# Kernel tuning notes

Hardware: AMD Instinct MI355X
Metric: run time of the kernel (lower is better)

## Reference

```python
import jax, jax.numpy as jnp
import numpy as np
from jax import lax

EPS = 0.1
MAX_ITER = 100
THRESH = 0.01
N = 4  # number of prompt ensembles


def _l2norm(x, axis):
    return x / jnp.linalg.norm(x, axis=axis, keepdims=True)


def sinkhorn(K, u, v, max_iter=MAX_ITER, thresh=THRESH):
    # K: [B, M, N], u: [B, M], v: [B, N]. Matches torch loop with early exit
    # on mean(|r - r0|) < thresh, done on-device via lax.while_loop.
    dt = K.dtype
    r0 = jnp.ones_like(u)
    c0 = jnp.ones_like(v)

    def cond(state):
        _, _, i, err = state
        return jnp.logical_and(i < max_iter, err >= thresh)

    def body(state):
        r, c, i, _ = state
        r_new = u / jnp.einsum('bmn,bn->bm', K, c)
        c_new = v / jnp.einsum('bmn,bm->bn', K, r_new)
        err = jnp.mean(jnp.abs(r_new - r))
        return (r_new, c_new, i + 1, err)

    r, c, _, _ = lax.while_loop(cond, body, (r0, c0, jnp.int32(0), jnp.asarray(jnp.inf, dt)))
    # T = outer(r, c) * K
    return r[:, :, None] * c[:, None, :] * K


def setup_inputs() -> dict:
    key = jax.random.key(0)
    k1, k2, k3 = jax.random.split(key, 3)
    M, b, d = 196, 32, 512
    n_cls = 1000
    return {
        'image_features': jax.random.normal(k1, (M, b, d), dtype=jnp.float32),
        'image_feature_pool': jax.random.normal(k2, (b, d), dtype=jnp.float32),
        'text_features': jax.random.normal(k3, (N * n_cls, d), dtype=jnp.float32),
        'logit_scale': jnp.asarray(np.log(1.0 / 0.07), dtype=jnp.float32),
    }


def reference(image_features, image_feature_pool, text_features, logit_scale):
    M, b, d = image_features.shape
    n_cls = text_features.shape[0] // N

    tf = text_features.reshape(N, n_cls, d)
    text_feature_pool = tf.mean(axis=0)

    imf = _l2norm(image_features, axis=2)          # [M, b, d]
    img_pool = _l2norm(image_feature_pool, axis=1)  # [b, d]
    tfn = _l2norm(tf, axis=2)                       # [N, n_cls, d]
    txt_pool = _l2norm(text_feature_pool, axis=1)   # [n_cls, d]

    # sim: [M, N, b, n_cls] -> [M, N, b*n_cls] -> [B, M, N]
    sim = jnp.einsum('mbd,ncd->mnbc', imf, tfn)
    sim = sim.reshape(M, N, b * n_cls).transpose(2, 0, 1)
    wdist = 1.0 - sim

    B = b * n_cls
    xx = jnp.full((B, M), 1.0 / M, dtype=sim.dtype)
    yy = jnp.full((B, N), 1.0 / N, dtype=sim.dtype)

    # torch.no_grad() around Sinkhorn -> stop gradients into the iteration
    K = jnp.exp(-lax.stop_gradient(wdist) / EPS)
    T = sinkhorn(K, xx, yy)

    sim_op = jnp.sum(T * sim, axis=(1, 2)).reshape(b, n_cls)

    ls = jnp.exp(logit_scale)
    logits = ls * (img_pool @ txt_pool.T)
    logits2 = 0.5 * (ls * sim_op) + 0.5 * logits
    return logits2
```

## Files before the change

### kernel.cpp

```cpp
#include <hip/hip_runtime.h>
#include <hip/hip_bf16.h>

#define MB 6272
#define NC 4000
#define DD 512
#define NCLS 1000
#define NB 32000
#define NITER 6
#define SK_STRIDE 68

typedef __attribute__((ext_vector_type(8))) short short8;
typedef __attribute__((ext_vector_type(4))) float f32x4;
typedef __attribute__((ext_vector_type(2))) float f32x2;

__device__ __forceinline__ float bflo(unsigned u) { return __builtin_bit_cast(float, u << 16); }
__device__ __forceinline__ float bfhi(unsigned u) { return __builtin_bit_cast(float, u & 0xFFFF0000u); }
__device__ __forceinline__ float frcp(float x) { return __builtin_amdgcn_rcpf(x); }

__device__ __forceinline__ unsigned short f2bf(float x) {
  unsigned u = __builtin_bit_cast(unsigned, x);
  u += 0x7FFFu + ((u >> 16) & 1u);
  return (unsigned short)(u >> 16);
}

__device__ __forceinline__ bool is_fp32_mode(const void* lsp) {
  const unsigned short u = *(const unsigned short*)lsp;
  const float v = __builtin_bit_cast(float, (unsigned)u << 16);
  return !(v > 2.55f && v < 2.77f);
}

__device__ __forceinline__ void gl_lds16(const unsigned short* g, unsigned short* l) {
  __builtin_amdgcn_global_load_lds(
      (const __attribute__((address_space(1))) void*)g,
      (__attribute__((address_space(3))) void*)l, 16, 0, 0);
}

__global__ __launch_bounds__(256) void prep(const void* __restrict__ imgf,
                                            const void* __restrict__ imgp,
                                            const void* __restrict__ txtf,
                                            const void* __restrict__ lsp,
                                            float* __restrict__ rnAT, float* __restrict__ rnB,
                                            float* __restrict__ imgpool,
                                            float* __restrict__ txtpool,
                                            unsigned short* __restrict__ Ab,
                                            unsigned short* __restrict__ Bb) {
  const bool f32 = is_fp32_mode(lsp);
  const int w = threadIdx.x >> 6;
  const int lane = threadIdx.x & 63;
  const int row = blockIdx.x * 4 + w;
  const int d0 = lane * 8;

  float v[8];
  auto load8f = [&](const void* base, int srow) {
    if (f32) {
      const float4 a = *reinterpret_cast<const float4*>((const float*)base + (size_t)srow * DD + d0);
      const float4 b = *reinterpret_cast<const float4*>((const float*)base + (size_t)srow * DD + d0 + 4);
      v[0] = a.x; v[1] = a.y; v[2] = a.z; v[3] = a.w;
      v[4] = b.x; v[5] = b.y; v[6] = b.z; v[7] = b.w;
    } else {
      const uint4 u = *reinterpret_cast<const uint4*>((const unsigned short*)base + (size_t)srow * DD + d0);
      v[0] = bflo(u.x); v[1] = bfhi(u.x); v[2] = bflo(u.y); v[3] = bfhi(u.y);
      v[4] = bflo(u.z); v[5] = bfhi(u.z); v[6] = bflo(u.w); v[7] = bfhi(u.w);
    }
  };

  int mode;
  unsigned short* dst16 = nullptr;
  float* dstf = nullptr;
  int outidx = 0;
  if (row < MB) {
    load8f(imgf, row); mode = 0; dst16 = Ab + (size_t)row * DD + d0;
    outidx = (row & 31) * 208 + (row >> 5);
  } else if (row < MB + NC) {
    const int j = row - MB;
    load8f(txtf, (j & 3) * NCLS + (j >> 2)); mode = 1;
    dst16 = Bb + (size_t)j * DD + d0; outidx = j;
  } else if (row < MB + NC + 32) {
    const int b = row - MB - NC;
    load8f(imgp, b); mode = 2; dstf = imgpool + (size_t)b * DD + d0;
  } else {
    const int cc = row - (MB + NC + 32);
    float acc8[8] = {0, 0, 0, 0, 0, 0, 0, 0};
#pragma unroll
    for (int n = 0; n < 4; ++n) {
      load8f(txtf, n * NCLS + cc);
#pragma unroll
      for (int i = 0; i < 8; ++i) acc8[i] += v[i];
    }
#pragma unroll
    for (int i = 0; i < 8; ++i) v[i] = acc8[i] * 0.25f;
    mode = 3; dstf = txtpool + (size_t)cc * DD + d0;
  }

  float ss = 0.f;
#pragma unroll
  for (int i = 0; i < 8; ++i) ss += v[i] * v[i];
#pragma unroll
  for (int off = 1; off < 64; off <<= 1) ss += __shfl_xor(ss, off);
  const float rn = rsqrtf(ss);

  if (mode <= 1) {
    union { uint4 u; unsigned short h[8]; } r;
#pragma unroll
    for (int i = 0; i < 8; ++i) r.h[i] = f2bf(v[i]);
    *reinterpret_cast<uint4*>(dst16) = r.u;
    if (lane == 0) (mode == 0 ? rnAT : rnB)[outidx] = rn;
  } else {
    float4 a, b;
    a.x = v[0] * rn; a.y = v[1] * rn; a.z = v[2] * rn; a.w = v[3] * rn;
    b.x = v[4] * rn; b.y = v[5] * rn; b.z = v[6] * rn; b.w = v[7] * rn;
    *reinterpret_cast<float4*>(dstf) = a;
    *reinterpret_cast<float4*>(dstf + 4) = b;
  }
}

__global__ __launch_bounds__(256, 4) void gemm_sink(const unsigned short* __restrict__ Ab,
                                                    const unsigned short* __restrict__ Bb,
                                                    const float* __restrict__ rnAT,
                                                    const float* __restrict__ rnB,
                                                    const float* __restrict__ imgpool,
                                                    const float* __restrict__ txtpool,
                                                    const void* __restrict__ lsp,
                                                    void* __restrict__ out) {
  __shared__ unsigned short shm[17408];
  __shared__ float rnAs[208];

  const int t = threadIdx.x;
  const int lane = t & 63;
  const int w = t >> 6;
  const int b = blockIdx.x;
  const int y = blockIdx.y;
  const int quad = lane >> 4, l16 = lane & 15;

  if (t < 208) rnAs[t] = rnAT[b * 208 + t];

  const unsigned short* asrc[3];
#pragma unroll
  for (int r = 0; r < 3; ++r) {
    const int g = r * 256 + t;
    const int rr = g >> 2;
    const int seg = g & 3;
    const int sg = (seg ^ (rr & 3)) * 8;
    asrc[r] = Ab + (size_t)(rr * 32 + b) * DD + sg;
  }
  const int xrr = 192 + (lane >> 2);
  const int xseg = lane & 3;
  const int xsg = (xseg ^ (xrr & 3)) * 8;
  const int xarow = xrr < 196 ? xrr : 195;
  const unsigned short* axsrc = Ab + (size_t)(xarow * 32 + b) * DD + xsg;
  const unsigned short* bsrc;
  {
    const int rr = t >> 2;
    const int seg = t & 3;
    const int sg = (seg ^ (rr & 3)) * 8;
    const int jg0 = y * 64 + rr;
    const int jg = jg0 < NC ? jg0 : NC - 1;
    bsrc = Bb + (size_t)jg * DD + sg;
  }

  f32x4 acc[13];
#pragma unroll
  for (int mt = 0; mt < 13; ++mt) acc[mt] = (f32x4)0.f;

  unsigned short* const buf0 = shm;
  unsigned short* const buf1 = shm + 8704;

  auto stage = [&](unsigned short* buf, int koff) {
#pragma unroll
    for (int r = 0; r < 3; ++r)
      gl_lds16(asrc[r] + koff, buf + (size_t)(r * 256 + w * 64) * 8);
    if (w == 0) gl_lds16(axsrc + koff, buf + (size_t)768 * 8);
    gl_lds16(bsrc + koff, buf + 6656 + (size_t)(w * 64) * 8);
  };

  auto compute = [&](const unsigned short* cb) {
    const unsigned short* Bsx = cb + 6656;
    const int rwb = w * 16 + l16;
    const short8 bf = *reinterpret_cast<const short8*>(&Bsx[rwb * 32 + (quad ^ (rwb & 3)) * 8]);
    __builtin_amdgcn_s_setprio(1);
#pragma unroll
    for (int mt = 0; mt < 13; ++mt) {
      const int rw = mt * 16 + l16;
      const short8 af = *reinterpret_cast<const short8*>(&cb[rw * 32 + (quad ^ (rw & 3)) * 8]);
      acc[mt] = __builtin_amdgcn_mfma_f32_16x16x32_bf16(af, bf, acc[mt], 0, 0, 0);
    }
    __builtin_amdgcn_s_setprio(0);
  };

  stage(buf0, 0);
  asm volatile("s_waitcnt vmcnt(0)" ::: "memory");
  __syncthreads();

#pragma unroll 1
  for (int kt = 0; kt < 16; kt += 2) {
    stage(buf1, (kt + 1) * 32);
    compute(buf0);
    asm volatile("s_waitcnt vmcnt(0)" ::: "memory");
    __builtin_amdgcn_s_barrier();
    if (kt < 14) stage(buf0, (kt + 2) * 32);
    compute(buf1);
    asm volatile("s_waitcnt vmcnt(0)" ::: "memory");
    __builtin_amdgcn_s_barrier();
  }

  {
    const int jl = w * 16 + l16;
    const int jg = y * 64 + jl;
    const float rb = jg < NC ? rnB[jg] : 1.0f;
#pragma unroll
    for (int mt = 0; mt < 13; ++mt) {
#pragma unroll
      for (int reg = 0; reg < 4; ++reg) {
        const int m = mt * 16 + quad * 4 + reg;
        if (m < 196) {
          const float sim = acc[mt][reg] * rnAs[m] * rb;
          shm[m * SK_STRIDE + jl] = f2bf(__expf(10.f * sim - 10.f));
        }
      }
    }
  }
  __syncthreads();

  const int pl = lane >> 4;
  const int sub = lane & 15;
  const int mstart = sub < 4 ? sub * 13 : 52 + (sub - 4) * 12;
  const int pcol = (w * 4 + pl) * 4;

  uint2 kk[13];
#pragma unroll
  for (int i = 0; i < 13; ++i) {
    const int m = mstart + i;
    const int mc = m < 196 ? m : 195;
    kk[i] = *reinterpret_cast<const uint2*>(&shm[mc * SK_STRIDE + pcol]);
  }

  f32x2 cA = {1.f, 1.f}, cB = {1.f, 1.f};
  for (int it = 0; it < NITER - 1; ++it) {
    f32x2 SA = {0.f, 0.f}, SB = {0.f, 0.f};
#pragma unroll
    for (int i = 0; i < 13; ++i) {
      if (i < 12 || sub < 4) {
        f32x2 kA = {bflo(kk[i].x), bfhi(kk[i].x)};
        f32x2 kB = {bflo(kk[i].y), bfhi(kk[i].y)};
        const f32x2 pr = kA * cA + kB * cB;
        const float rv = (1.0f / 196.0f) * frcp(pr.x + pr.y);
        const f32x2 rvv = {rv, rv};
        SA += kA * rvv;
        SB += kB * rvv;
      }
    }
    SA.x += __shfl_xor(SA.x, 1); SA.x += __shfl_xor(SA.x, 2); SA.x += __shfl_xor(SA.x, 4); SA.x += __shfl_xor(SA.x, 8);
    SA.y += __shfl_xor(SA.y, 1); SA.y += __shfl_xor(SA.y, 2); SA.y += __shfl_xor(SA.y, 4); SA.y += __shfl_xor(SA.y, 8);
    SB.x += __shfl_xor(SB.x, 1); SB.x += __shfl_xor(SB.x, 2); SB.x += __shfl_xor(SB.x, 4); SB.x += __shfl_xor(SB.x, 8);
    SB.y += __shfl_xor(SB.y, 1); SB.y += __shfl_xor(SB.y, 2); SB.y += __shfl_xor(SB.y, 4); SB.y += __shfl_xor(SB.y, 8);
    cA.x = 0.25f * frcp(SA.x); cA.y = 0.25f * frcp(SA.y);
    cB.x = 0.25f * frcp(SB.x); cB.y = 0.25f * frcp(SB.y);
  }

  f32x2 SA = {0.f, 0.f}, SB = {0.f, 0.f}, WA = {0.f, 0.f}, WB = {0.f, 0.f};
#pragma unroll
  for (int i = 0; i < 13; ++i) {
    if (i < 12 || sub < 4) {
      f32x2 kA = {bflo(kk[i].x), bfhi(kk[i].x)};
      f32x2 kB = {bflo(kk[i].y), bfhi(kk[i].y)};
      const f32x2 pr = kA * cA + kB * cB;
      const float rv = (1.0f / 196.0f) * frcp(pr.x + pr.y);
      const f32x2 rvv = {rv, rv};
      const f32x2 tA = kA * rvv, tB = kB * rvv;
      SA += tA; SB += tB;
      const f32x2 lgA = {__logf(kA.x), __logf(kA.y)};
      const f32x2 lgB = {__logf(kB.x), __logf(kB.y)};
      const f32x2 one = {1.f, 1.f}, tenth = {0.1f, 0.1f};
      WA += tA * (one + tenth * lgA);
      WB += tB * (one + tenth * lgB);
    }
  }
  SA.x += __shfl_xor(SA.x, 1); SA.x += __shfl_xor(SA.x, 2); SA.x += __shfl_xor(SA.x, 4); SA.x += __shfl_xor(SA.x, 8);
  SA.y += __shfl_xor(SA.y, 1); SA.y += __shfl_xor(SA.y, 2); SA.y += __shfl_xor(SA.y, 4); SA.y += __shfl_xor(SA.y, 8);
  SB.x += __shfl_xor(SB.x, 1); SB.x += __shfl_xor(SB.x, 2); SB.x += __shfl_xor(SB.x, 4); SB.x += __shfl_xor(SB.x, 8);
  SB.y += __shfl_xor(SB.y, 1); SB.y += __shfl_xor(SB.y, 2); SB.y += __shfl_xor(SB.y, 4); SB.y += __shfl_xor(SB.y, 8);
  WA.x += __shfl_xor(WA.x, 1); WA.x += __shfl_xor(WA.x, 2); WA.x += __shfl_xor(WA.x, 4); WA.x += __shfl_xor(WA.x, 8);
  WA.y += __shfl_xor(WA.y, 1); WA.y += __shfl_xor(WA.y, 2); WA.y += __shfl_xor(WA.y, 4); WA.y += __shfl_xor(WA.y, 8);
  WB.x += __shfl_xor(WB.x, 1); WB.x += __shfl_xor(WB.x, 2); WB.x += __shfl_xor(WB.x, 4); WB.x += __shfl_xor(WB.x, 8);
  WB.y += __shfl_xor(WB.y, 1); WB.y += __shfl_xor(WB.y, 2); WB.y += __shfl_xor(WB.y, 4); WB.y += __shfl_xor(WB.y, 8);
  const float simop = (0.25f * frcp(SA.x)) * WA.x + (0.25f * frcp(SA.y)) * WA.y +
                      (0.25f * frcp(SB.x)) * WB.x + (0.25f * frcp(SB.y)) * WB.y;

  const int cg = y * 16 + (w * 4 + pl);
  const int cgc = cg < NCLS ? cg : NCLS - 1;
  const float4* ip4 = reinterpret_cast<const float4*>(imgpool + (size_t)b * DD);
  const float4* tp4 = reinterpret_cast<const float4*>(txtpool + (size_t)cgc * DD);
  float dot = 0.f;
#pragma unroll
  for (int i = 0; i < 8; ++i) {
    const float4 a = ip4[sub * 8 + i];
    const float4 v = tp4[sub * 8 + i];
    dot += (a.x * v.x + a.y * v.y) + (a.z * v.z + a.w * v.w);
  }
  dot += __shfl_xor(dot, 1); dot += __shfl_xor(dot, 2); dot += __shfl_xor(dot, 4); dot += __shfl_xor(dot, 8);

  if (sub == 0 && cg < NCLS) {
    const bool f32 = is_fp32_mode(lsp);
    const float lsv = f32 ? *(const float*)lsp : bflo(*(const unsigned short*)lsp);
    const float val = 0.5f * __expf(lsv) * (simop + dot);
    const int p = b * NCLS + cg;
    if (f32) ((float*)out)[p] = val;
    else ((unsigned short*)out)[p] = f2bf(val);
  }
}

extern "C" void kernel_launch(void* const* d_in, const int* in_sizes, int n_in,
                              void* d_out, int out_size, void* d_ws, size_t ws_size,
                              hipStream_t stream) {
  const void* imgf = d_in[0];
  const void* imgp = d_in[1];
  const void* txtf = d_in[2];
  const void* lsp  = d_in[3];

  const size_t need = (size_t)32 * 208 * 4 + NC * 4 + 32 * DD * 4 + NCLS * DD * 4 +
                      (size_t)MB * DD * 2 + (size_t)NC * DD * 2;
  const bool ok = (n_in == 4) && in_sizes[0] == MB * DD && in_sizes[1] == 32 * DD &&
                  in_sizes[2] == NC * DD && in_sizes[3] == 1 && out_size == NB &&
                  ws_size >= need;
  if (!ok) return;

  char* w = (char*)d_ws;
  float* rnAT = (float*)w;                 w += (size_t)32 * 208 * 4;
  float* rnB = (float*)w;                  w += NC * 4;
  float* imgpool = (float*)w;              w += 32 * DD * 4;
  float* txtpool = (float*)w;              w += NCLS * DD * 4;
  unsigned short* Ab = (unsigned short*)w; w += (size_t)MB * DD * 2;
  unsigned short* Bb = (unsigned short*)w; w += (size_t)NC * DD * 2;

  prep<<<dim3(2826), dim3(256), 0, stream>>>(imgf, imgp, txtf, lsp, rnAT, rnB,
                                             imgpool, txtpool, Ab, Bb);
  gemm_sink<<<dim3(32, 63), dim3(256), 0, stream>>>(Ab, Bb, rnAT, rnB, imgpool,
                                                    txtpool, lsp, d_out);
}
```

Measured before the change: 143.8 us.

## Split GEMM tile across waves by M rows instead of N columns

Each wave now owns a slice of the 13 M-tiles (4, 3, 3 and 3) across all four 16-column N-tiles, instead of all 13 M-tiles for one N-tile. This cuts redundant LDS reads of A fragments: each wave reads at most 4 A fragments plus 4 B fragments per k-step, rather than 13 A plus 1. Accumulator count rises from 13 to 16 per lane, so the launch-bounds occupancy hint drops from 4 to 3 blocks. Wave 0 does one more M-tile than the others, which unbalances the work.

```diff
diff --git a/kernel.cpp b/kernel.cpp
--- a/kernel.cpp
+++ b/kernel.cpp
@@ -114,7 +114,7 @@
   }
 }
 
-__global__ __launch_bounds__(256, 4) void gemm_sink(const unsigned short* __restrict__ Ab,
+__global__ __launch_bounds__(256, 3) void gemm_sink(const unsigned short* __restrict__ Ab,
                                                     const unsigned short* __restrict__ Bb,
                                                     const float* __restrict__ rnAT,
                                                     const float* __restrict__ rnB,
@@ -131,6 +131,9 @@
   const int b = blockIdx.x;
   const int y = blockIdx.y;
   const int quad = lane >> 4, l16 = lane & 15;
+
+  const int mbase = (w == 0) ? 0 : (3 * w + 1);
+  const int nmt = (w == 0) ? 4 : 3;
 
   if (t < 208) rnAs[t] = rnAT[b * 208 + t];
 
@@ -158,9 +161,11 @@
     bsrc = Bb + (size_t)jg * DD + sg;
   }
 
-  f32x4 acc[13];
-#pragma unroll
-  for (int mt = 0; mt < 13; ++mt) acc[mt] = (f32x4)0.f;
+  f32x4 acc[4][4];
+#pragma unroll
+  for (int i = 0; i < 4; ++i)
+#pragma unroll
+    for (int jt = 0; jt < 4; ++jt) acc[i][jt] = (f32x4)0.f;
 
   unsigned short* const buf0 = shm;
   unsigned short* const buf1 = shm + 8704;
@@ -175,14 +180,22 @@
 
   auto compute = [&](const unsigned short* cb) {
     const unsigned short* Bsx = cb + 6656;
-    const int rwb = w * 16 + l16;
-    const short8 bf = *reinterpret_cast<const short8*>(&Bsx[rwb * 32 + (quad ^ (rwb & 3)) * 8]);
+    short8 bfr[4];
+#pragma unroll
+    for (int jt = 0; jt < 4; ++jt) {
+      const int rwb = jt * 16 + l16;
+      bfr[jt] = *reinterpret_cast<const short8*>(&Bsx[rwb * 32 + (quad ^ (rwb & 3)) * 8]);
+    }
     __builtin_amdgcn_s_setprio(1);
 #pragma unroll
-    for (int mt = 0; mt < 13; ++mt) {
-      const int rw = mt * 16 + l16;
-      const short8 af = *reinterpret_cast<const short8*>(&cb[rw * 32 + (quad ^ (rw & 3)) * 8]);
-      acc[mt] = __builtin_amdgcn_mfma_f32_16x16x32_bf16(af, bf, acc[mt], 0, 0, 0);
+    for (int i = 0; i < 4; ++i) {
+      if (i < nmt) {
+        const int rw = (mbase + i) * 16 + l16;
+        const short8 af = *reinterpret_cast<const short8*>(&cb[rw * 32 + (quad ^ (rw & 3)) * 8]);
+#pragma unroll
+        for (int jt = 0; jt < 4; ++jt)
+          acc[i][jt] = __builtin_amdgcn_mfma_f32_16x16x32_bf16(af, bfr[jt], acc[i][jt], 0, 0, 0);
+      }
     }
     __builtin_amdgcn_s_setprio(0);
   };
@@ -204,17 +217,26 @@
   }
 
   {
-    const int jl = w * 16 + l16;
-    const int jg = y * 64 + jl;
-    const float rb = jg < NC ? rnB[jg] : 1.0f;
-#pragma unroll
-    for (int mt = 0; mt < 13; ++mt) {
-#pragma unroll
-      for (int reg = 0; reg < 4; ++reg) {
-        const int m = mt * 16 + quad * 4 + reg;
-        if (m < 196) {
-          const float sim = acc[mt][reg] * rnAs[m] * rb;
-          shm[m * SK_STRIDE + jl] = f2bf(__expf(10.f * sim - 10.f));
+    float rbv[4];
+#pragma unroll
+    for (int jt = 0; jt < 4; ++jt) {
+      const int jg = y * 64 + jt * 16 + l16;
+      rbv[jt] = jg < NC ? rnB[jg] : 1.0f;
+    }
+#pragma unroll
+    for (int i = 0; i < 4; ++i) {
+      if (i < nmt) {
+#pragma unroll
+        for (int jt = 0; jt < 4; ++jt) {
+          const int jl = jt * 16 + l16;
+#pragma unroll
+          for (int reg = 0; reg < 4; ++reg) {
+            const int m = (mbase + i) * 16 + quad * 4 + reg;
+            if (m < 196) {
+              const float sim = acc[i][jt][reg] * rnAs[m] * rbv[jt];
+              shm[m * SK_STRIDE + jl] = f2bf(__expf(10.f * sim - 10.f));
+            }
+          }
         }
       }
     }
```

Measured after the change: 140.8 us. -2.1%, faster.
